# Kernel optimization log

Measured on AMD Instinct MI355X. Metric: run time of the kernel, lower is better.

## Reference

```python
import jax, jax.numpy as jnp
import numpy as np

B, D, K, L, H = 16384, 1024, 512, 128, 64  # batch, input_dim, num_components, latent_dim, phi hidden
EPS = 1e-9


def setup_inputs() -> dict:
    key = jax.random.key(0)
    k0, k1, k2, k3 = jax.random.split(key, 4)
    # small scales keep squared distances O(1-10) so exp(-d2) is non-degenerate
    x = jax.random.normal(k0, (B, D), jnp.float32) * 0.03
    z_samples = jax.random.normal(k1, (K, L), jnp.float32)
    W1 = jax.random.normal(k2, (L, H), jnp.float32) * (1.0 / np.sqrt(L)).astype(np.float32)
    b1 = jnp.zeros((H,), jnp.float32)
    W2 = jax.random.normal(k3, (H, D), jnp.float32) * 0.01
    b2 = jnp.zeros((D,), jnp.float32)
    return {"x": x, "z_samples": z_samples, "W1": W1, "b1": b1, "W2": W2, "b2": b2}


def reference(x, z_samples, W1, b1, W2, b2):
    # PhiNet: Linear -> ReLU -> Linear, applied to all components at once
    phi = jnp.maximum(z_samples @ W1 + b1, 0.0) @ W2 + b2          # (K, D)
    # ||x - phi_k||^2 for all (k, b) via GEMM expansion (fuses the per-component loop)
    sq = (jnp.sum(phi * phi, axis=-1)[:, None]
          + jnp.sum(x * x, axis=-1)[None, :]
          - 2.0 * (phi @ x.T))                                      # (K, B)
    lik = jnp.exp(-sq)                                              # (K, B)
    # weights = 1/K; sum_k w * lik = mean over K
    mixture_ll = jnp.log(jnp.mean(lik, axis=0) + EPS)               # (B,)
    return mixture_ll.mean()
```

## Files before the change

kernel.cpp:

```cpp
#include <hip/hip_runtime.h>
#include <hip/hip_bf16.h>
#include <stdint.h>

#define N_B   16384
#define D_DIM 1024
#define K_K   512
#define L_DIM 128
#define H_DIM 64
#define SX    1032

typedef __attribute__((ext_vector_type(8))) short short8;
typedef __attribute__((ext_vector_type(4))) float f32x4;

__device__ __forceinline__ unsigned short f2bf(float f) {
    union { float f; unsigned int u; } c; c.f = f;
    unsigned int u = c.u;
    unsigned int r = (u + 0x7FFFu + ((u >> 16) & 1u)) >> 16;
    return (unsigned short)r;
}

__device__ __forceinline__ unsigned int pk2(float a, float b) {
    __hip_bfloat162 t = __float22bfloat162_rn(make_float2(a, b));
    union { __hip_bfloat162 h; unsigned int u; } c; c.h = t;
    return c.u;
}

__global__ __launch_bounds__(256) void prep_kernel(
    const float* __restrict__ z, const float* __restrict__ W1,
    const float* __restrict__ b1, const float* __restrict__ W2,
    const float* __restrict__ b2, unsigned short* __restrict__ W2bf,
    unsigned short* __restrict__ h_bf, float* __restrict__ phi2) {
    __shared__ float zsh[8][L_DIM];
    __shared__ float hsh[8][H_DIM];
    __shared__ float redp[4][8];
    const int tid = threadIdx.x;
    const int k0 = blockIdx.x * 8;

    {
        int i = blockIdx.x * 256 + tid;
        float4 v = ((const float4*)W2)[i];
        uint2 o = make_uint2(pk2(v.x, v.y), pk2(v.z, v.w));
        *(uint2*)(W2bf + i * 4) = o;
    }
#pragma unroll
    for (int c = 0; c < 4; ++c) {
        int idx = c * 256 + tid;
        zsh[idx >> 7][idx & 127] = z[k0 * L_DIM + idx];
    }
    __syncthreads();
    {
        const int j = tid & 63, kk = tid >> 6;
        float bb = b1[j];
        float s0 = bb, s1 = bb;
        for (int l = 0; l < L_DIM; ++l) {
            float w = W1[l * H_DIM + j];
            s0 += zsh[kk][l] * w;
            s1 += zsh[kk + 4][l] * w;
        }
        float h0 = fmaxf(s0, 0.0f), h1 = fmaxf(s1, 0.0f);
        hsh[kk][j] = h0; hsh[kk + 4][j] = h1;
        h_bf[(k0 + kk) * H_DIM + j]     = f2bf(h0);
        h_bf[(k0 + kk + 4) * H_DIM + j] = f2bf(h1);
    }
    __syncthreads();
    float ss[8] = {0.f, 0.f, 0.f, 0.f, 0.f, 0.f, 0.f, 0.f};
#pragma unroll
    for (int c = 0; c < 4; ++c) {
        int d = c * 256 + tid;
        float bb = b2[d];
        float a[8];
#pragma unroll
        for (int kk = 0; kk < 8; ++kk) a[kk] = bb;
        for (int j = 0; j < H_DIM; ++j) {
            float w = W2[j * D_DIM + d];
#pragma unroll
            for (int kk = 0; kk < 8; ++kk) a[kk] += hsh[kk][j] * w;
        }
#pragma unroll
        for (int kk = 0; kk < 8; ++kk) ss[kk] += a[kk] * a[kk];
    }
    const int lane = tid & 63, wv = tid >> 6;
#pragma unroll
    for (int kk = 0; kk < 8; ++kk) {
        float v = ss[kk];
#pragma unroll
        for (int o = 1; o < 64; o <<= 1) v += __shfl_xor(v, o, 64);
        if (lane == 0) redp[wv][kk] = v;
    }
    __syncthreads();
    if (tid < 8) phi2[k0 + tid] = redp[0][tid] + redp[1][tid] + redp[2][tid] + redp[3][tid];
}

__global__ __launch_bounds__(256) void main_kernel(
    const float* __restrict__ x, const unsigned short* __restrict__ W2bf,
    const unsigned short* __restrict__ h_bf, const float* __restrict__ phi2,
    const float* __restrict__ b2, float* __restrict__ out) {
    __shared__ __align__(16) unsigned short x_bf[32 * SX];
    __shared__ __align__(16) unsigned short u_tile[32 * 72];
    __shared__ float phi2s[K_K];
    __shared__ float x2s[32], xb2s[32];
    __shared__ float red[4][32];

    const int tid = threadIdx.x;
    const int wv  = tid >> 6;
    const int l   = tid & 63;
    const int lm  = l & 15;
    const int q   = l >> 4;
    const int n0  = blockIdx.x * 32;

    float4 b2r[4];
#pragma unroll
    for (int sub = 0; sub < 4; ++sub)
        b2r[sub] = ((const float4*)b2)[sub * 64 + l];

    phi2s[tid]       = phi2[tid];
    phi2s[256 + tid] = phi2[256 + tid];

    float x2a[8], xba[8];
#pragma unroll
    for (int batch = 0; batch < 2; ++batch) {
        const int r0 = wv * 8 + batch * 4;
        float4 xv[16];
#pragma unroll
        for (int s = 0; s < 4; ++s)
#pragma unroll
            for (int sub = 0; sub < 4; ++sub)
                xv[s * 4 + sub] = *(const float4*)(x + (size_t)(n0 + r0 + s) * D_DIM + sub * 256 + l * 4);
#pragma unroll
        for (int s = 0; s < 4; ++s) {
            float s2 = 0.f, sb = 0.f;
#pragma unroll
            for (int sub = 0; sub < 4; ++sub) {
                float4 v = xv[s * 4 + sub];
                s2 += v.x*v.x + v.y*v.y + v.z*v.z + v.w*v.w;
                sb += v.x*b2r[sub].x + v.y*b2r[sub].y + v.z*b2r[sub].z + v.w*b2r[sub].w;
                uint2 o = make_uint2(pk2(v.x, v.y), pk2(v.z, v.w));
                *(uint2*)&x_bf[(r0 + s) * SX + sub * 256 + l * 4] = o;
            }
            x2a[batch * 4 + s] = s2; xba[batch * 4 + s] = sb;
        }
    }
#pragma unroll
    for (int s = 0; s < 8; ++s) {
        float a = x2a[s], b = xba[s];
#pragma unroll
        for (int o = 1; o < 64; o <<= 1) { a += __shfl_xor(a, o, 64); b += __shfl_xor(b, o, 64); }
        if (l == 0) { x2s[wv * 8 + s] = a; xb2s[wv * 8 + s] = b; }
    }
    __syncthreads();

    const unsigned short* w2row = W2bf + (size_t)(wv * 16 + lm) * D_DIM + q * 8;
    short8 wf[8];
#pragma unroll
    for (int p = 0; p < 8; ++p)
        wf[p] = *(const short8*)(w2row + p * 32);
    f32x4 c1[2] = {};
#pragma unroll
    for (int ks = 0; ks < 32; ++ks) {
        const int k0 = ks * 32 + q * 8;
        short8 bw = wf[ks & 7];
        if (ks < 24)
            wf[ks & 7] = *(const short8*)(w2row + (ks + 8) * 32);
        short8 a0 = *(const short8*)&x_bf[lm * SX + k0];
        short8 a1 = *(const short8*)&x_bf[(16 + lm) * SX + k0];
        c1[0] = __builtin_amdgcn_mfma_f32_16x16x32_bf16(a0, bw, c1[0], 0, 0, 0);
        c1[1] = __builtin_amdgcn_mfma_f32_16x16x32_bf16(a1, bw, c1[1], 0, 0, 0);
    }
#pragma unroll
    for (int i = 0; i < 2; ++i)
#pragma unroll
        for (int r = 0; r < 4; ++r)
            u_tile[(i * 16 + q * 4 + r) * 72 + wv * 16 + lm] = f2bf(c1[i][r]);
    __syncthreads();

    f32x4 acc[8][2] = {};
#pragma unroll
    for (int ks = 0; ks < 2; ++ks) {
        const int ko = ks * 32 + q * 8;
        short8 bfr[2];
#pragma unroll
        for (int j = 0; j < 2; ++j)
            bfr[j] = *(const short8*)&u_tile[(j * 16 + lm) * 72 + ko];
#pragma unroll
        for (int i = 0; i < 8; ++i) {
            short8 a = *(const short8*)(h_bf + (size_t)(wv * 128 + i * 16 + lm) * H_DIM + ko);
#pragma unroll
            for (int j = 0; j < 2; ++j)
                acc[i][j] = __builtin_amdgcn_mfma_f32_16x16x32_bf16(a, bfr[j], acc[i][j], 0, 0, 0);
        }
    }
    float xn0 = x2s[lm]      - 2.f * xb2s[lm];
    float xn1 = x2s[16 + lm] - 2.f * xb2s[16 + lm];
    float cs0 = 0.f, cs1 = 0.f;
#pragma unroll
    for (int i = 0; i < 8; ++i) {
#pragma unroll
        for (int r = 0; r < 4; ++r) {
            float p2 = phi2s[wv * 128 + i * 16 + q * 4 + r];
            cs0 += __expf(-(p2 + xn0 - 2.f * acc[i][0][r]));
            cs1 += __expf(-(p2 + xn1 - 2.f * acc[i][1][r]));
        }
    }
    cs0 += __shfl_xor(cs0, 16, 64); cs0 += __shfl_xor(cs0, 32, 64);
    cs1 += __shfl_xor(cs1, 16, 64); cs1 += __shfl_xor(cs1, 32, 64);
    if (l < 16) { red[wv][l] = cs0; red[wv][16 + l] = cs1; }
    __syncthreads();
    if (tid < 32) {
        float row_lik = red[0][tid] + red[1][tid] + red[2][tid] + red[3][tid];
        float lg = __logf(row_lik * (1.0f / (float)K_K) + 1e-9f);
        lg += __shfl_xor(lg, 1, 64);
        lg += __shfl_xor(lg, 2, 64);
        lg += __shfl_xor(lg, 4, 64);
        lg += __shfl_xor(lg, 8, 64);
        lg += __shfl_xor(lg, 16, 64);
        if (tid == 0) atomicAdd(out, lg * (1.0f / (float)N_B));
    }
}

extern "C" void kernel_launch(void* const* d_in, const int* in_sizes, int n_in,
                              void* d_out, int out_size, void* d_ws, size_t ws_size,
                              hipStream_t stream) {
    const float* x  = (const float*)d_in[0];
    const float* z  = (const float*)d_in[1];
    const float* W1 = (const float*)d_in[2];
    const float* b1 = (const float*)d_in[3];
    const float* W2 = (const float*)d_in[4];
    const float* b2 = (const float*)d_in[5];

    char* ws = (char*)d_ws;
    unsigned short* W2bf = (unsigned short*)(ws);
    unsigned short* h_bf = (unsigned short*)(ws + 131072);
    float*          phi2 = (float*)(ws + 196608);

    hipMemsetAsync(d_out, 0, sizeof(float), stream);
    prep_kernel<<<64, 256, 0, stream>>>(z, W1, b1, W2, b2, W2bf, h_bf, phi2);
    main_kernel<<<N_B / 32, 256, 0, stream>>>(x, W2bf, h_bf, phi2, b2, (float*)d_out);
}
```

Measured before the change: 144.2 us.

## Double-buffer x chunks in LDS to overlap global loads with MFMA

```diff
diff --git a/kernel.cpp b/kernel.cpp
--- a/kernel.cpp
+++ b/kernel.cpp
@@ -7,7 +7,7 @@
 #define K_K   512
 #define L_DIM 128
 #define H_DIM 64
-#define SX    1032
+#define SC    264
 
 typedef __attribute__((ext_vector_type(8))) short short8;
 typedef __attribute__((ext_vector_type(4))) float f32x4;
@@ -95,7 +95,7 @@
     const float* __restrict__ x, const unsigned short* __restrict__ W2bf,
     const unsigned short* __restrict__ h_bf, const float* __restrict__ phi2,
     const float* __restrict__ b2, float* __restrict__ out) {
-    __shared__ __align__(16) unsigned short x_bf[32 * SX];
+    __shared__ __align__(16) unsigned short xc[2][32 * SC];
     __shared__ __align__(16) unsigned short u_tile[32 * 72];
     __shared__ float phi2s[K_K];
     __shared__ float x2s[32], xb2s[32];
@@ -110,36 +110,68 @@
 
     float4 b2r[4];
 #pragma unroll
-    for (int sub = 0; sub < 4; ++sub)
-        b2r[sub] = ((const float4*)b2)[sub * 64 + l];
+    for (int ch = 0; ch < 4; ++ch)
+        b2r[ch] = ((const float4*)b2)[ch * 64 + l];
 
     phi2s[tid]       = phi2[tid];
     phi2s[256 + tid] = phi2[256 + tid];
 
     float x2a[8], xba[8];
-#pragma unroll
-    for (int batch = 0; batch < 2; ++batch) {
-        const int r0 = wv * 8 + batch * 4;
-        float4 xv[16];
-#pragma unroll
-        for (int s = 0; s < 4; ++s)
-#pragma unroll
-            for (int sub = 0; sub < 4; ++sub)
-                xv[s * 4 + sub] = *(const float4*)(x + (size_t)(n0 + r0 + s) * D_DIM + sub * 256 + l * 4);
-#pragma unroll
-        for (int s = 0; s < 4; ++s) {
-            float s2 = 0.f, sb = 0.f;
-#pragma unroll
-            for (int sub = 0; sub < 4; ++sub) {
-                float4 v = xv[s * 4 + sub];
-                s2 += v.x*v.x + v.y*v.y + v.z*v.z + v.w*v.w;
-                sb += v.x*b2r[sub].x + v.y*b2r[sub].y + v.z*b2r[sub].z + v.w*b2r[sub].w;
+    {
+        float4 xv[8];
+#pragma unroll
+        for (int s = 0; s < 8; ++s)
+            xv[s] = *(const float4*)(x + (size_t)(n0 + wv * 8 + s) * D_DIM + l * 4);
+#pragma unroll
+        for (int s = 0; s < 8; ++s) {
+            float4 v = xv[s];
+            x2a[s] = v.x*v.x + v.y*v.y + v.z*v.z + v.w*v.w;
+            xba[s] = v.x*b2r[0].x + v.y*b2r[0].y + v.z*b2r[0].z + v.w*b2r[0].w;
+            uint2 o = make_uint2(pk2(v.x, v.y), pk2(v.z, v.w));
+            *(uint2*)&xc[0][(wv * 8 + s) * SC + l * 4] = o;
+        }
+    }
+    __syncthreads();
+
+    f32x4 c1[2] = {};
+#pragma unroll
+    for (int ch = 0; ch < 4; ++ch) {
+        const int cur = ch & 1;
+        short8 wf[8];
+#pragma unroll
+        for (int p = 0; p < 8; ++p)
+            wf[p] = *(const short8*)(W2bf + (size_t)(wv * 16 + lm) * D_DIM + ch * 256 + p * 32 + q * 8);
+        float4 xv[8];
+        if (ch < 3) {
+#pragma unroll
+            for (int s = 0; s < 8; ++s)
+                xv[s] = *(const float4*)(x + (size_t)(n0 + wv * 8 + s) * D_DIM + (ch + 1) * 256 + l * 4);
+        }
+#pragma unroll
+        for (int ks = 0; ks < 8; ++ks) {
+            const int k0 = ks * 32 + q * 8;
+            short8 a0 = *(const short8*)&xc[cur][lm * SC + k0];
+            short8 a1 = *(const short8*)&xc[cur][(16 + lm) * SC + k0];
+            c1[0] = __builtin_amdgcn_mfma_f32_16x16x32_bf16(a0, wf[ks], c1[0], 0, 0, 0);
+            c1[1] = __builtin_amdgcn_mfma_f32_16x16x32_bf16(a1, wf[ks], c1[1], 0, 0, 0);
+        }
+        if (ch < 3) {
+#pragma unroll
+            for (int s = 0; s < 8; ++s) {
+                float4 v = xv[s];
+                x2a[s] += v.x*v.x + v.y*v.y + v.z*v.z + v.w*v.w;
+                xba[s] += v.x*b2r[ch + 1].x + v.y*b2r[ch + 1].y + v.z*b2r[ch + 1].z + v.w*b2r[ch + 1].w;
                 uint2 o = make_uint2(pk2(v.x, v.y), pk2(v.z, v.w));
-                *(uint2*)&x_bf[(r0 + s) * SX + sub * 256 + l * 4] = o;
+                *(uint2*)&xc[cur ^ 1][(wv * 8 + s) * SC + l * 4] = o;
             }
-            x2a[batch * 4 + s] = s2; xba[batch * 4 + s] = sb;
-        }
-    }
+            __syncthreads();
+        }
+    }
+#pragma unroll
+    for (int i = 0; i < 2; ++i)
+#pragma unroll
+        for (int r = 0; r < 4; ++r)
+            u_tile[(i * 16 + q * 4 + r) * 72 + wv * 16 + lm] = f2bf(c1[i][r]);
 #pragma unroll
     for (int s = 0; s < 8; ++s) {
         float a = x2a[s], b = xba[s];
@@ -147,30 +179,6 @@
         for (int o = 1; o < 64; o <<= 1) { a += __shfl_xor(a, o, 64); b += __shfl_xor(b, o, 64); }
         if (l == 0) { x2s[wv * 8 + s] = a; xb2s[wv * 8 + s] = b; }
     }
-    __syncthreads();
-
-    const unsigned short* w2row = W2bf + (size_t)(wv * 16 + lm) * D_DIM + q * 8;
-    short8 wf[8];
-#pragma unroll
-    for (int p = 0; p < 8; ++p)
-        wf[p] = *(const short8*)(w2row + p * 32);
-    f32x4 c1[2] = {};
-#pragma unroll
-    for (int ks = 0; ks < 32; ++ks) {
-        const int k0 = ks * 32 + q * 8;
-        short8 bw = wf[ks & 7];
-        if (ks < 24)
-            wf[ks & 7] = *(const short8*)(w2row + (ks + 8) * 32);
-        short8 a0 = *(const short8*)&x_bf[lm * SX + k0];
-        short8 a1 = *(const short8*)&x_bf[(16 + lm) * SX + k0];
-        c1[0] = __builtin_amdgcn_mfma_f32_16x16x32_bf16(a0, bw, c1[0], 0, 0, 0);
-        c1[1] = __builtin_amdgcn_mfma_f32_16x16x32_bf16(a1, bw, c1[1], 0, 0, 0);
-    }
-#pragma unroll
-    for (int i = 0; i < 2; ++i)
-#pragma unroll
-        for (int r = 0; r < 4; ++r)
-            u_tile[(i * 16 + q * 4 + r) * 72 + wv * 16 + lm] = f2bf(c1[i][r]);
     __syncthreads();
 
     f32x4 acc[8][2] = {};
```

Measured after the change: 154.1 us. 6.9% more time.

## Split fused main kernel into separate projection and likelihood kernels

Applied to the files above, without the earlier changes.

```diff
diff --git a/kernel.cpp b/kernel.cpp
--- a/kernel.cpp
+++ b/kernel.cpp
@@ -91,43 +91,36 @@
     if (tid < 8) phi2[k0 + tid] = redp[0][tid] + redp[1][tid] + redp[2][tid] + redp[3][tid];
 }
 
-__global__ __launch_bounds__(256) void main_kernel(
+__global__ __launch_bounds__(256) void u_kernel(
     const float* __restrict__ x, const unsigned short* __restrict__ W2bf,
-    const unsigned short* __restrict__ h_bf, const float* __restrict__ phi2,
-    const float* __restrict__ b2, float* __restrict__ out) {
-    __shared__ __align__(16) unsigned short x_bf[32 * SX];
-    __shared__ __align__(16) unsigned short u_tile[32 * 72];
-    __shared__ float phi2s[K_K];
-    __shared__ float x2s[32], xb2s[32];
-    __shared__ float red[4][32];
+    const float* __restrict__ b2, float* __restrict__ u_out,
+    float* __restrict__ xn_out) {
+    __shared__ __align__(16) unsigned short x_bf[16 * SX];
 
     const int tid = threadIdx.x;
     const int wv  = tid >> 6;
     const int l   = tid & 63;
     const int lm  = l & 15;
     const int q   = l >> 4;
-    const int n0  = blockIdx.x * 32;
+    const int n0  = blockIdx.x * 16;
 
     float4 b2r[4];
 #pragma unroll
     for (int sub = 0; sub < 4; ++sub)
         b2r[sub] = ((const float4*)b2)[sub * 64 + l];
 
-    phi2s[tid]       = phi2[tid];
-    phi2s[256 + tid] = phi2[256 + tid];
-
-    float x2a[8], xba[8];
+    float x2a[4], xba[4];
 #pragma unroll
     for (int batch = 0; batch < 2; ++batch) {
-        const int r0 = wv * 8 + batch * 4;
-        float4 xv[16];
-#pragma unroll
-        for (int s = 0; s < 4; ++s)
+        const int r0 = wv * 4 + batch * 2;
+        float4 xv[8];
+#pragma unroll
+        for (int s = 0; s < 2; ++s)
 #pragma unroll
             for (int sub = 0; sub < 4; ++sub)
                 xv[s * 4 + sub] = *(const float4*)(x + (size_t)(n0 + r0 + s) * D_DIM + sub * 256 + l * 4);
 #pragma unroll
-        for (int s = 0; s < 4; ++s) {
+        for (int s = 0; s < 2; ++s) {
             float s2 = 0.f, sb = 0.f;
 #pragma unroll
             for (int sub = 0; sub < 4; ++sub) {
@@ -137,15 +130,15 @@
                 uint2 o = make_uint2(pk2(v.x, v.y), pk2(v.z, v.w));
                 *(uint2*)&x_bf[(r0 + s) * SX + sub * 256 + l * 4] = o;
             }
-            x2a[batch * 4 + s] = s2; xba[batch * 4 + s] = sb;
-        }
-    }
-#pragma unroll
-    for (int s = 0; s < 8; ++s) {
+            x2a[batch * 2 + s] = s2; xba[batch * 2 + s] = sb;
+        }
+    }
+#pragma unroll
+    for (int s = 0; s < 4; ++s) {
         float a = x2a[s], b = xba[s];
 #pragma unroll
         for (int o = 1; o < 64; o <<= 1) { a += __shfl_xor(a, o, 64); b += __shfl_xor(b, o, 64); }
-        if (l == 0) { x2s[wv * 8 + s] = a; xb2s[wv * 8 + s] = b; }
+        if (l == 0) xn_out[n0 + wv * 4 + s] = a - 2.f * b;
     }
     __syncthreads();
 
@@ -154,43 +147,68 @@
 #pragma unroll
     for (int p = 0; p < 8; ++p)
         wf[p] = *(const short8*)(w2row + p * 32);
-    f32x4 c1[2] = {};
+    f32x4 c1 = {};
 #pragma unroll
     for (int ks = 0; ks < 32; ++ks) {
-        const int k0 = ks * 32 + q * 8;
         short8 bw = wf[ks & 7];
         if (ks < 24)
             wf[ks & 7] = *(const short8*)(w2row + (ks + 8) * 32);
-        short8 a0 = *(const short8*)&x_bf[lm * SX + k0];
-        short8 a1 = *(const short8*)&x_bf[(16 + lm) * SX + k0];
-        c1[0] = __builtin_amdgcn_mfma_f32_16x16x32_bf16(a0, bw, c1[0], 0, 0, 0);
-        c1[1] = __builtin_amdgcn_mfma_f32_16x16x32_bf16(a1, bw, c1[1], 0, 0, 0);
-    }
-#pragma unroll
-    for (int i = 0; i < 2; ++i)
-#pragma unroll
-        for (int r = 0; r < 4; ++r)
-            u_tile[(i * 16 + q * 4 + r) * 72 + wv * 16 + lm] = f2bf(c1[i][r]);
+        short8 a0 = *(const short8*)&x_bf[lm * SX + ks * 32 + q * 8];
+        c1 = __builtin_amdgcn_mfma_f32_16x16x32_bf16(a0, bw, c1, 0, 0, 0);
+    }
+#pragma unroll
+    for (int r = 0; r < 4; ++r)
+        u_out[(size_t)(n0 + q * 4 + r) * H_DIM + wv * 16 + lm] = c1[r];
+}
+
+__global__ __launch_bounds__(256) void s_kernel(
+    const float* __restrict__ u, const float* __restrict__ xn_g,
+    const unsigned short* __restrict__ h_bf, const float* __restrict__ phi2,
+    float* __restrict__ out) {
+    __shared__ float phi2s[K_K];
+    __shared__ float red[4][32];
+
+    const int tid = threadIdx.x;
+    const int wv  = tid >> 6;
+    const int l   = tid & 63;
+    const int lm  = l & 15;
+    const int q   = l >> 4;
+    const int n0  = blockIdx.x * 32;
+
+    phi2s[tid]       = phi2[tid];
+    phi2s[256 + tid] = phi2[256 + tid];
+
+    short8 bfr[2][2];
+#pragma unroll
+    for (int ks = 0; ks < 2; ++ks)
+#pragma unroll
+        for (int j = 0; j < 2; ++j) {
+            const float* up = u + (size_t)(n0 + j * 16 + lm) * H_DIM + ks * 32 + q * 8;
+            float4 p0 = *(const float4*)up;
+            float4 p1 = *(const float4*)(up + 4);
+            union { short8 s8; unsigned int uu[4]; } pb;
+            pb.uu[0] = pk2(p0.x, p0.y);
+            pb.uu[1] = pk2(p0.z, p0.w);
+            pb.uu[2] = pk2(p1.x, p1.y);
+            pb.uu[3] = pk2(p1.z, p1.w);
+            bfr[ks][j] = pb.s8;
+        }
     __syncthreads();
 
     f32x4 acc[8][2] = {};
 #pragma unroll
     for (int ks = 0; ks < 2; ++ks) {
         const int ko = ks * 32 + q * 8;
-        short8 bfr[2];
-#pragma unroll
-        for (int j = 0; j < 2; ++j)
-            bfr[j] = *(const short8*)&u_tile[(j * 16 + lm) * 72 + ko];
 #pragma unroll
         for (int i = 0; i < 8; ++i) {
             short8 a = *(const short8*)(h_bf + (size_t)(wv * 128 + i * 16 + lm) * H_DIM + ko);
 #pragma unroll
             for (int j = 0; j < 2; ++j)
-                acc[i][j] = __builtin_amdgcn_mfma_f32_16x16x32_bf16(a, bfr[j], acc[i][j], 0, 0, 0);
-        }
-    }
-    float xn0 = x2s[lm]      - 2.f * xb2s[lm];
-    float xn1 = x2s[16 + lm] - 2.f * xb2s[16 + lm];
+                acc[i][j] = __builtin_amdgcn_mfma_f32_16x16x32_bf16(a, bfr[ks][j], acc[i][j], 0, 0, 0);
+        }
+    }
+    float xn0 = xn_g[n0 + lm];
+    float xn1 = xn_g[n0 + 16 + lm];
     float cs0 = 0.f, cs1 = 0.f;
 #pragma unroll
     for (int i = 0; i < 8; ++i) {
@@ -231,8 +249,11 @@
     unsigned short* W2bf = (unsigned short*)(ws);
     unsigned short* h_bf = (unsigned short*)(ws + 131072);
     float*          phi2 = (float*)(ws + 196608);
+    float*          u    = (float*)(ws + 200704);
+    float*          xn   = (float*)(ws + 200704 + 4194304);
 
     hipMemsetAsync(d_out, 0, sizeof(float), stream);
     prep_kernel<<<64, 256, 0, stream>>>(z, W1, b1, W2, b2, W2bf, h_bf, phi2);
-    main_kernel<<<N_B / 32, 256, 0, stream>>>(x, W2bf, h_bf, phi2, b2, (float*)d_out);
-}
+    u_kernel<<<N_B / 16, 256, 0, stream>>>(x, W2bf, b2, u, xn);
+    s_kernel<<<N_B / 32, 256, 0, stream>>>(u, xn, h_bf, phi2, (float*)d_out);
+}
```

Result: slower. 160.0 us (+11.0%).

## Precompute bf16 x and row norms in prep kernel, DMA x tiles into LDS

Applied to the files above, without the earlier changes.

```diff
diff --git a/kernel.cpp b/kernel.cpp
--- a/kernel.cpp
+++ b/kernel.cpp
@@ -11,6 +11,7 @@
 
 typedef __attribute__((ext_vector_type(8))) short short8;
 typedef __attribute__((ext_vector_type(4))) float f32x4;
+typedef unsigned int u32;
 
 __device__ __forceinline__ unsigned short f2bf(float f) {
     union { float f; unsigned int u; } c; c.f = f;
@@ -25,22 +26,51 @@
     return c.u;
 }
 
+__device__ __forceinline__ void dma16(const void* g, void* l) {
+    __builtin_amdgcn_global_load_lds(
+        (const __attribute__((address_space(1))) u32*)g,
+        (__attribute__((address_space(3))) u32*)l, 16, 0, 0);
+}
+
 __global__ __launch_bounds__(256) void prep_kernel(
-    const float* __restrict__ z, const float* __restrict__ W1,
-    const float* __restrict__ b1, const float* __restrict__ W2,
-    const float* __restrict__ b2, unsigned short* __restrict__ W2bf,
-    unsigned short* __restrict__ h_bf, float* __restrict__ phi2) {
+    const float* __restrict__ x, const float* __restrict__ z,
+    const float* __restrict__ W1, const float* __restrict__ b1,
+    const float* __restrict__ W2, const float* __restrict__ b2,
+    unsigned short* __restrict__ W2bf, unsigned short* __restrict__ h_bf,
+    float* __restrict__ phi2, unsigned short* __restrict__ xbf,
+    float* __restrict__ x2g, float* __restrict__ xb2g) {
+    const int tid = threadIdx.x;
+    const int wv  = tid >> 6;
+    const int l   = tid & 63;
+
+    {
+        const int row = blockIdx.x * 4 + wv;
+        const float4* xr = (const float4*)(x + (size_t)row * D_DIM);
+        uint2* xo = (uint2*)(xbf + (size_t)row * D_DIM);
+        float s2 = 0.f, sb = 0.f;
+#pragma unroll
+        for (int s = 0; s < 4; ++s) {
+            float4 v = xr[s * 64 + l];
+            float4 bb = ((const float4*)b2)[s * 64 + l];
+            s2 += v.x*v.x + v.y*v.y + v.z*v.z + v.w*v.w;
+            sb += v.x*bb.x + v.y*bb.y + v.z*bb.z + v.w*bb.w;
+            xo[s * 64 + l] = make_uint2(pk2(v.x, v.y), pk2(v.z, v.w));
+        }
+#pragma unroll
+        for (int o = 1; o < 64; o <<= 1) { s2 += __shfl_xor(s2, o, 64); sb += __shfl_xor(sb, o, 64); }
+        if (l == 0) { x2g[row] = s2; xb2g[row] = sb; }
+    }
+
+    if (blockIdx.x >= 64) return;
+
     __shared__ float zsh[8][L_DIM];
     __shared__ float hsh[8][H_DIM];
     __shared__ float redp[4][8];
-    const int tid = threadIdx.x;
     const int k0 = blockIdx.x * 8;
-
     {
         int i = blockIdx.x * 256 + tid;
         float4 v = ((const float4*)W2)[i];
-        uint2 o = make_uint2(pk2(v.x, v.y), pk2(v.z, v.w));
-        *(uint2*)(W2bf + i * 4) = o;
+        *(uint2*)(W2bf + i * 4) = make_uint2(pk2(v.x, v.y), pk2(v.z, v.w));
     }
 #pragma unroll
     for (int c = 0; c < 4; ++c) {
@@ -52,10 +82,10 @@
         const int j = tid & 63, kk = tid >> 6;
         float bb = b1[j];
         float s0 = bb, s1 = bb;
-        for (int l = 0; l < L_DIM; ++l) {
-            float w = W1[l * H_DIM + j];
-            s0 += zsh[kk][l] * w;
-            s1 += zsh[kk + 4][l] * w;
+        for (int ll = 0; ll < L_DIM; ++ll) {
+            float w = W1[ll * H_DIM + j];
+            s0 += zsh[kk][ll] * w;
+            s1 += zsh[kk + 4][ll] * w;
         }
         float h0 = fmaxf(s0, 0.0f), h1 = fmaxf(s1, 0.0f);
         hsh[kk][j] = h0; hsh[kk + 4][j] = h1;
@@ -79,26 +109,25 @@
 #pragma unroll
         for (int kk = 0; kk < 8; ++kk) ss[kk] += a[kk] * a[kk];
     }
-    const int lane = tid & 63, wv = tid >> 6;
 #pragma unroll
     for (int kk = 0; kk < 8; ++kk) {
         float v = ss[kk];
 #pragma unroll
         for (int o = 1; o < 64; o <<= 1) v += __shfl_xor(v, o, 64);
-        if (lane == 0) redp[wv][kk] = v;
+        if (l == 0) redp[wv][kk] = v;
     }
     __syncthreads();
     if (tid < 8) phi2[k0 + tid] = redp[0][tid] + redp[1][tid] + redp[2][tid] + redp[3][tid];
 }
 
 __global__ __launch_bounds__(256) void main_kernel(
-    const float* __restrict__ x, const unsigned short* __restrict__ W2bf,
+    const unsigned short* __restrict__ xbf, const unsigned short* __restrict__ W2bf,
     const unsigned short* __restrict__ h_bf, const float* __restrict__ phi2,
-    const float* __restrict__ b2, float* __restrict__ out) {
+    const float* __restrict__ x2g, const float* __restrict__ xb2g,
+    float* __restrict__ out) {
     __shared__ __align__(16) unsigned short x_bf[32 * SX];
     __shared__ __align__(16) unsigned short u_tile[32 * 72];
     __shared__ float phi2s[K_K];
-    __shared__ float x2s[32], xb2s[32];
     __shared__ float red[4][32];
 
     const int tid = threadIdx.x;
@@ -108,45 +137,14 @@
     const int q   = l >> 4;
     const int n0  = blockIdx.x * 32;
 
-    float4 b2r[4];
-#pragma unroll
-    for (int sub = 0; sub < 4; ++sub)
-        b2r[sub] = ((const float4*)b2)[sub * 64 + l];
-
+    const char* xsrc = (const char*)xbf + (size_t)(n0 + wv * 8) * 2048 + (size_t)l * 16;
+#pragma unroll
+    for (int r = 0; r < 8; ++r)
+#pragma unroll
+        for (int c = 0; c < 2; ++c)
+            dma16(xsrc + r * 2048 + c * 1024, &x_bf[(wv * 8 + r) * SX + c * 512]);
     phi2s[tid]       = phi2[tid];
     phi2s[256 + tid] = phi2[256 + tid];
-
-    float x2a[8], xba[8];
-#pragma unroll
-    for (int batch = 0; batch < 2; ++batch) {
-        const int r0 = wv * 8 + batch * 4;
-        float4 xv[16];
-#pragma unroll
-        for (int s = 0; s < 4; ++s)
-#pragma unroll
-            for (int sub = 0; sub < 4; ++sub)
-                xv[s * 4 + sub] = *(const float4*)(x + (size_t)(n0 + r0 + s) * D_DIM + sub * 256 + l * 4);
-#pragma unroll
-        for (int s = 0; s < 4; ++s) {
-            float s2 = 0.f, sb = 0.f;
-#pragma unroll
-            for (int sub = 0; sub < 4; ++sub) {
-                float4 v = xv[s * 4 + sub];
-                s2 += v.x*v.x + v.y*v.y + v.z*v.z + v.w*v.w;
-                sb += v.x*b2r[sub].x + v.y*b2r[sub].y + v.z*b2r[sub].z + v.w*b2r[sub].w;
-                uint2 o = make_uint2(pk2(v.x, v.y), pk2(v.z, v.w));
-                *(uint2*)&x_bf[(r0 + s) * SX + sub * 256 + l * 4] = o;
-            }
-            x2a[batch * 4 + s] = s2; xba[batch * 4 + s] = sb;
-        }
-    }
-#pragma unroll
-    for (int s = 0; s < 8; ++s) {
-        float a = x2a[s], b = xba[s];
-#pragma unroll
-        for (int o = 1; o < 64; o <<= 1) { a += __shfl_xor(a, o, 64); b += __shfl_xor(b, o, 64); }
-        if (l == 0) { x2s[wv * 8 + s] = a; xb2s[wv * 8 + s] = b; }
-    }
     __syncthreads();
 
     const unsigned short* w2row = W2bf + (size_t)(wv * 16 + lm) * D_DIM + q * 8;
@@ -189,8 +187,8 @@
                 acc[i][j] = __builtin_amdgcn_mfma_f32_16x16x32_bf16(a, bfr[j], acc[i][j], 0, 0, 0);
         }
     }
-    float xn0 = x2s[lm]      - 2.f * xb2s[lm];
-    float xn1 = x2s[16 + lm] - 2.f * xb2s[16 + lm];
+    float xn0 = x2g[n0 + lm]      - 2.f * xb2g[n0 + lm];
+    float xn1 = x2g[n0 + 16 + lm] - 2.f * xb2g[n0 + 16 + lm];
     float cs0 = 0.f, cs1 = 0.f;
 #pragma unroll
     for (int i = 0; i < 8; ++i) {
@@ -231,8 +229,13 @@
     unsigned short* W2bf = (unsigned short*)(ws);
     unsigned short* h_bf = (unsigned short*)(ws + 131072);
     float*          phi2 = (float*)(ws + 196608);
+    float*          x2g  = (float*)(ws + 200704);
+    float*          xb2g = (float*)(ws + 266240);
+    unsigned short* xbf  = (unsigned short*)(ws + 393216);
 
     hipMemsetAsync(d_out, 0, sizeof(float), stream);
-    prep_kernel<<<64, 256, 0, stream>>>(z, W1, b1, W2, b2, W2bf, h_bf, phi2);
-    main_kernel<<<N_B / 32, 256, 0, stream>>>(x, W2bf, h_bf, phi2, b2, (float*)d_out);
-}
+    prep_kernel<<<N_B / 4, 256, 0, stream>>>(x, z, W1, b1, W2, b2,
+                                             W2bf, h_bf, phi2, xbf, x2g, xb2g);
+    main_kernel<<<N_B / 32, 256, 0, stream>>>(xbf, W2bf, h_bf, phi2, x2g, xb2g,
+                                              (float*)d_out);
+}
```

Result: slower. 152.2 us (+5.5%).
